# Kernel optimization log

Hardware: AMD Instinct MI355X
Metric: run time of the kernel (lower is better)

## Reference

```python
import jax, jax.numpy as jnp
import numpy as np

B, T, N, H = 256, 128, 512, 128  # batch, timesteps, input_size (driving series), hidden


def setup_inputs() -> dict:
    key = jax.random.key(0)
    ks = jax.random.split(key, 7)
    p = lambda k, shape: (jax.random.normal(k, shape, dtype=jnp.float32) * 0.05)
    return {
        "X": jax.random.normal(ks[0], (B, T, N), dtype=jnp.float32),
        # attention linear: in_features = 2H + T, out_features = 1 (stored as a vector + scalar bias)
        "attn_w": p(ks[1], (2 * H + T,)),
        "attn_b": p(ks[2], ()),
        # LSTM cell params, PyTorch layout/gate order (i, f, g, o)
        "w_ih": p(ks[3], (4 * H, N)),
        "w_hh": p(ks[4], (4 * H, H)),
        "b_ih": p(ks[5], (4 * H,)),
        "b_hh": p(ks[6], (4 * H,)),
    }


def reference(X, attn_w, attn_b, w_ih, w_hh, b_ih, b_hh):
    Bn, Tn, Nn = X.shape
    Hh = w_hh.shape[1]
    # split the single attention weight row into the h / s / X-row pieces of the concat
    w_h, w_s, w_x = attn_w[:Hh], attn_w[Hh:2 * Hh], attn_w[2 * Hh:]
    Xp = jnp.swapaxes(X, 1, 2)            # [B, N, T]  (X.permute(0,2,1))
    x_score = Xp @ w_x                    # [B, N], time-invariant part of attention logits

    def step(carry, x_t):                 # x_t: [B, N] = X[:, t, :]
        h, c = carry
        # logits[b,i] = w_h.h[b] + w_s.c[b] + w_x.Xp[b,i] + b  (== Linear on the concat)
        score = x_score + (h @ w_h + c @ w_s + attn_b)[:, None]   # [B, N]
        alpha = jax.nn.softmax(score, axis=1)
        x_tilde = alpha * x_t                                      # [B, N]
        gates = x_tilde @ w_ih.T + h @ w_hh.T + b_ih + b_hh        # [B, 4H]
        i, f, g, o = jnp.split(gates, 4, axis=1)
        c_new = jax.nn.sigmoid(f) * c + jax.nn.sigmoid(i) * jnp.tanh(g)
        h_new = jax.nn.sigmoid(o) * jnp.tanh(c_new)
        return (h_new, c_new), (x_tilde, h_new)

    h0 = jnp.zeros((Bn, Hh), X.dtype)
    (_, _), (Xt, Xe) = jax.lax.scan(step, (h0, h0), jnp.swapaxes(X, 0, 1))
    # scan stacks along time -> [T, B, .]; return [B, T, .]
    return jnp.swapaxes(Xt, 0, 1), jnp.swapaxes(Xe, 0, 1)
```

## Files before the change

### kernel.cpp

```cpp
#include <hip/hip_runtime.h>
#include <hip/hip_bf16.h>

#define Bb 256
#define Tt 128
#define Nn 512
#define Hh 128

typedef __attribute__((ext_vector_type(4))) float floatx4;
typedef __attribute__((ext_vector_type(8))) short short8;

__device__ __forceinline__ unsigned short f2bf(float f) {
  unsigned u = __float_as_uint(f);
  u += 0x7fffu + ((u >> 16) & 1u);
  return (unsigned short)(u >> 16);
}

__device__ __forceinline__ float sigmoid_fast(float x) {
  return __builtin_amdgcn_rcpf(1.f + __expf(-x));
}
__device__ __forceinline__ float tanh_fast(float x) {
  float e = __expf(2.f * x);
  return 1.f - 2.f * __builtin_amdgcn_rcpf(e + 1.f);
}

__device__ __forceinline__ void lds_barrier() {
  asm volatile("s_waitcnt lgkmcnt(0)" ::: "memory");
  __builtin_amdgcn_s_barrier();
  asm volatile("" ::: "memory");
}

__device__ __forceinline__ void async_load16(const void* g, void* lds) {
  __builtin_amdgcn_global_load_lds(
      (const __attribute__((address_space(1))) unsigned int*)g,
      (__attribute__((address_space(3))) unsigned int*)lds, 16, 0, 0);
}

__global__ void prep_kernel(const float* __restrict__ w_ih,
                            const float* __restrict__ b_ih,
                            const float* __restrict__ b_hh,
                            unsigned short* __restrict__ wb,
                            float* __restrict__ bias) {
  int i = blockIdx.x * 256 + threadIdx.x;
  if (i < 4 * Hh * Nn) wb[i] = f2bf(w_ih[i]);
  if (i < 4 * Hh) bias[i] = b_ih[i] + b_hh[i];
}

__global__ __launch_bounds__(512) void alpha_kernel(const float* __restrict__ X,
                                                    const float* __restrict__ attn_w,
                                                    float* __restrict__ alpha) {
  int b = blockIdx.x;
  int n = threadIdx.x;
  const float* Xb = X + (size_t)b * Tt * Nn + n;
  float acc = 0.f;
#pragma unroll 8
  for (int t = 0; t < Tt; ++t)
    acc = fmaf(Xb[(size_t)t * Nn], attn_w[2 * Hh + t], acc);

  __shared__ float red[512];
  red[n] = acc;
  __syncthreads();
  for (int s = 256; s > 0; s >>= 1) {
    if (n < s) red[n] = fmaxf(red[n], red[n + s]);
    __syncthreads();
  }
  float m = red[0];
  __syncthreads();
  float e = __expf(acc - m);
  red[n] = e;
  __syncthreads();
  for (int s = 256; s > 0; s >>= 1) {
    if (n < s) red[n] += red[n + s];
    __syncthreads();
  }
  alpha[(size_t)b * Nn + n] = e / red[0];
}

__global__ __launch_bounds__(256) void scale_kernel(const float* __restrict__ X,
                                                    const float* __restrict__ alpha,
                                                    float* __restrict__ Xt,
                                                    unsigned short* __restrict__ xtb) {
  size_t i = (size_t)blockIdx.x * 256 + threadIdx.x;
  size_t e = i * 4;
  int n = (int)(e & (Nn - 1));
  int brow = (int)(e >> 9);
  int b = brow >> 7;
  float4 x = ((const float4*)X)[i];
  float4 a = *(const float4*)(alpha + (size_t)b * Nn + n);
  float4 y;
  y.x = x.x * a.x; y.y = x.y * a.y; y.z = x.z * a.z; y.w = x.w * a.w;
  ((float4*)Xt)[i] = y;
  ushort4 u;
  u.x = f2bf(y.x); u.y = f2bf(y.y); u.z = f2bf(y.z); u.w = f2bf(y.w);
  ((ushort4*)xtb)[i] = u;
}

#define GBK 64

__global__ __launch_bounds__(256) void gemm_bt(const unsigned short* __restrict__ A,
                                               const unsigned short* __restrict__ Bw,
                                               const float* __restrict__ bias,
                                               float* __restrict__ C) {
  __shared__ __align__(16) unsigned short As[128 * 64];
  __shared__ __align__(16) unsigned short Bs[128 * 64];
  const int K = 512, NO = 512;
  int tid = threadIdx.x;
  int lane = tid & 63;
  int wave = tid >> 6;
  int wm = wave & 1, wn = wave >> 1;
  int l15 = lane & 15;
  int quad = lane >> 4;
  int mtile = blockIdx.x, ntile = blockIdx.y;

  floatx4 acc[4][4];
#pragma unroll
  for (int i = 0; i < 4; ++i)
#pragma unroll
    for (int j = 0; j < 4; ++j) acc[i][j] = (floatx4){0.f, 0.f, 0.f, 0.f};

  int lr = lane >> 3;
  int lc = (lane & 7) ^ lr;
  const size_t lane_goff = (size_t)lr * K + lc * 8;
  const size_t abase = (size_t)mtile * 128 * K + lane_goff;
  const size_t bbase = (size_t)ntile * 128 * K + lane_goff;
  int sw = (quad ^ (l15 & 7)) * 8;

  for (int kb = 0; kb < K; kb += GBK) {
#pragma unroll
    for (int slot = 0; slot < 4; ++slot) {
      int r0 = slot * 32 + wave * 8;
      async_load16(A + abase + (size_t)r0 * K + kb, &As[r0 * 64]);
      async_load16(Bw + bbase + (size_t)r0 * K + kb, &Bs[r0 * 64]);
    }
    __syncthreads();
#pragma unroll
    for (int kh = 0; kh < 2; ++kh) {
      int sc = sw ^ (kh * 32);
      short8 af[4], bf[4];
#pragma unroll
      for (int i = 0; i < 4; ++i)
        af[i] = *(const short8*)(&As[(wm * 64 + i * 16 + l15) * 64 + sc]);
#pragma unroll
      for (int j = 0; j < 4; ++j)
        bf[j] = *(const short8*)(&Bs[(wn * 64 + j * 16 + l15) * 64 + sc]);
#pragma unroll
      for (int i = 0; i < 4; ++i)
#pragma unroll
        for (int j = 0; j < 4; ++j)
          acc[i][j] = __builtin_amdgcn_mfma_f32_16x16x32_bf16(af[i], bf[j], acc[i][j], 0, 0, 0);
    }
    __syncthreads();
  }

  int m0 = mtile * 128 + wm * 64;
  int n0 = ntile * 128 + wn * 64;
#pragma unroll
  for (int j = 0; j < 4; ++j) {
    int col = n0 + j * 16 + l15;
    float bsum = bias[col];
#pragma unroll
    for (int i = 0; i < 4; ++i) {
      int row = m0 + i * 16 + quad * 4;
#pragma unroll
      for (int r = 0; r < 4; ++r)
        C[(size_t)(row + r) * NO + col] = acc[i][j][r] + bsum;
    }
  }
}

__global__ __launch_bounds__(512, 1) void lstm_kernel(const float* __restrict__ G,
                                                      const float* __restrict__ w_hh,
                                                      float* __restrict__ Xe) {
  int b = blockIdx.x;
  int tid = threadIdx.x;
  int w = tid >> 6;
  int lane = tid & 63;
  int l15 = lane & 15;
  int quad = lane >> 4;

  short8 bfr[4][4];
#pragma unroll
  for (int f = 0; f < 4; ++f) {
    int n = f * 128 + w * 16 + l15;
    const float* src = w_hh + (size_t)n * 128;
#pragma unroll
    for (int kf = 0; kf < 4; ++kf) {
      int k0 = kf * 32 + quad * 8;
      float4 lo = *(const float4*)(src + k0);
      float4 hi = *(const float4*)(src + k0 + 4);
      short8 v;
      v[0] = (short)f2bf(lo.x); v[1] = (short)f2bf(lo.y);
      v[2] = (short)f2bf(lo.z); v[3] = (short)f2bf(lo.w);
      v[4] = (short)f2bf(hi.x); v[5] = (short)f2bf(hi.y);
      v[6] = (short)f2bf(hi.z); v[7] = (short)f2bf(hi.w);
      bfr[f][kf] = v;
    }
  }

  __shared__ __align__(16) unsigned short h_sh[2][128];
  if (tid < 128) h_sh[0][tid] = 0;
  __syncthreads();

  const float* Gb = G + (size_t)b * Tt * 512;
  float* Xeb = Xe + (size_t)b * Tt * Hh;

  int goff[4];
#pragma unroll
  for (int f = 0; f < 4; ++f) goff[f] = f * 128 + w * 16 + l15;

  float gcur[4], gnext[4];
#pragma unroll
  for (int f = 0; f < 4; ++f) gcur[f] = Gb[goff[f]];
#pragma unroll
  for (int f = 0; f < 4; ++f) gnext[f] = Gb[512 + goff[f]];

  float c0 = 0.f;
  int j0 = w * 16 + l15;

  for (int t = 0; t < Tt; ++t) {
    int cur = t & 1;
    const unsigned short* hp = h_sh[cur];
    short8 af[4];
#pragma unroll
    for (int kf = 0; kf < 4; ++kf)
      af[kf] = *(const short8*)(hp + kf * 32 + quad * 8);

    floatx4 acc[4];
#pragma unroll
    for (int f = 0; f < 4; ++f)
      acc[f] = (floatx4){gcur[f], gcur[f], gcur[f], gcur[f]};

#pragma unroll
    for (int f = 0; f < 4; ++f) gcur[f] = gnext[f];
    if (t + 2 < Tt) {
      const float* Gt2 = Gb + (size_t)(t + 2) * 512;
#pragma unroll
      for (int f = 0; f < 4; ++f) gnext[f] = Gt2[goff[f]];
    }

#pragma unroll
    for (int kf = 0; kf < 4; ++kf)
#pragma unroll
      for (int f = 0; f < 4; ++f)
        acc[f] = __builtin_amdgcn_mfma_f32_16x16x32_bf16(af[kf], bfr[f][kf], acc[f], 0, 0, 0);

    float si = sigmoid_fast(acc[0][0]);
    float sf = sigmoid_fast(acc[1][0]);
    float tg = tanh_fast(acc[2][0]);
    float so = sigmoid_fast(acc[3][0]);

    c0 = sf * c0 + si * tg;
    float hv = so * tanh_fast(c0);

    if (quad == 0) {
      Xeb[(size_t)t * Hh + j0] = hv;
      h_sh[cur ^ 1][j0] = f2bf(hv);
    }
    lds_barrier();
  }
}

extern "C" void kernel_launch(void* const* d_in, const int* in_sizes, int n_in,
                              void* d_out, int out_size, void* d_ws, size_t ws_size,
                              hipStream_t stream) {
  const float* X      = (const float*)d_in[0];
  const float* attn_w = (const float*)d_in[1];
  const float* w_ih   = (const float*)d_in[3];
  const float* w_hh   = (const float*)d_in[4];
  const float* b_ih   = (const float*)d_in[5];
  const float* b_hh   = (const float*)d_in[6];

  float* Xt = (float*)d_out;
  float* Xe = (float*)d_out + (size_t)Bb * Tt * Nn;

  char* ws = (char*)d_ws;
  float*          alpha = (float*)(ws);
  float*          bias  = (float*)(ws + 524288);
  unsigned short* wb    = (unsigned short*)(ws + 526336);
  unsigned short* xtb   = (unsigned short*)(ws + 1050624);
  float*          G     = (float*)(ws + 34605056);

  prep_kernel<<<dim3(1024), dim3(256), 0, stream>>>(w_ih, b_ih, b_hh, wb, bias);
  alpha_kernel<<<dim3(Bb), dim3(512), 0, stream>>>(X, attn_w, alpha);
  scale_kernel<<<dim3(16384), dim3(256), 0, stream>>>(X, alpha, Xt, xtb);
  gemm_bt<<<dim3(256, 4), dim3(256), 0, stream>>>(xtb, wb, bias, G);
  lstm_kernel<<<dim3(Bb), dim3(512), 0, stream>>>(G, w_hh, Xe);
}
```

Baseline: 276.9 us.

## Replace MFMA recurrent matvec with fp16 dot2 and quad DPP reduction

```diff
diff --git a/kernel.cpp b/kernel.cpp
--- a/kernel.cpp
+++ b/kernel.cpp
@@ -8,6 +8,7 @@
 
 typedef __attribute__((ext_vector_type(4))) float floatx4;
 typedef __attribute__((ext_vector_type(8))) short short8;
+typedef _Float16 h2v_t __attribute__((ext_vector_type(2)));
 
 __device__ __forceinline__ unsigned short f2bf(float f) {
   unsigned u = __float_as_uint(f);
@@ -33,6 +34,25 @@
   __builtin_amdgcn_global_load_lds(
       (const __attribute__((address_space(1))) unsigned int*)g,
       (__attribute__((address_space(3))) unsigned int*)lds, 16, 0, 0);
+}
+
+#if __has_builtin(__builtin_amdgcn_fdot2)
+#define FDOT2(a, b, c) __builtin_amdgcn_fdot2((a), (b), (c), false)
+#else
+__device__ __forceinline__ float fdot2_sw(h2v_t a, h2v_t b, float c) {
+  return fmaf((float)a.x, (float)b.x, fmaf((float)a.y, (float)b.y, (c)));
+}
+#define FDOT2(a, b, c) fdot2_sw((a), (b), (c))
+#endif
+
+template <int CTRL>
+__device__ __forceinline__ float qperm(float x) {
+#if __has_builtin(__builtin_amdgcn_update_dpp)
+  return __uint_as_float((unsigned)__builtin_amdgcn_update_dpp(
+      0, (int)__float_as_uint(x), CTRL, 0xf, 0xf, true));
+#else
+  return __shfl_xor(x, CTRL == 0xB1 ? 1 : 2, 64);
+#endif
 }
 
 __global__ void prep_kernel(const float* __restrict__ w_ih,
@@ -172,88 +192,75 @@
                                                       float* __restrict__ Xe) {
   int b = blockIdx.x;
   int tid = threadIdx.x;
-  int w = tid >> 6;
-  int lane = tid & 63;
-  int l15 = lane & 15;
-  int quad = lane >> 4;
-
-  short8 bfr[4][4];
+  int u = tid >> 2;
+  int q = tid & 3;
+
+  h2v_t wreg[4][16];
 #pragma unroll
   for (int f = 0; f < 4; ++f) {
-    int n = f * 128 + w * 16 + l15;
-    const float* src = w_hh + (size_t)n * 128;
-#pragma unroll
-    for (int kf = 0; kf < 4; ++kf) {
-      int k0 = kf * 32 + quad * 8;
-      float4 lo = *(const float4*)(src + k0);
-      float4 hi = *(const float4*)(src + k0 + 4);
-      short8 v;
-      v[0] = (short)f2bf(lo.x); v[1] = (short)f2bf(lo.y);
-      v[2] = (short)f2bf(lo.z); v[3] = (short)f2bf(lo.w);
-      v[4] = (short)f2bf(hi.x); v[5] = (short)f2bf(hi.y);
-      v[6] = (short)f2bf(hi.z); v[7] = (short)f2bf(hi.w);
-      bfr[f][kf] = v;
-    }
-  }
-
-  __shared__ __align__(16) unsigned short h_sh[2][128];
-  if (tid < 128) h_sh[0][tid] = 0;
-  __syncthreads();
-
-  const float* Gb = G + (size_t)b * Tt * 512;
+    const float4* wr = (const float4*)(w_hh + ((size_t)(f * 128 + u) * 128 + q * 32));
+#pragma unroll
+    for (int i = 0; i < 8; ++i) {
+      float4 v = wr[i];
+      wreg[f][2 * i]     = (h2v_t){(_Float16)v.x, (_Float16)v.y};
+      wreg[f][2 * i + 1] = (h2v_t){(_Float16)v.z, (_Float16)v.w};
+    }
+  }
+
+  __shared__ __align__(16) unsigned short h2[2][128];
+  if (tid < 128) h2[0][tid] = 0;
+  __syncthreads();
+
+  const float* Gb = G + (size_t)b * Tt * 512 + q * 128 + u;
   float* Xeb = Xe + (size_t)b * Tt * Hh;
 
-  int goff[4];
-#pragma unroll
-  for (int f = 0; f < 4; ++f) goff[f] = f * 128 + w * 16 + l15;
-
-  float gcur[4], gnext[4];
-#pragma unroll
-  for (int f = 0; f < 4; ++f) gcur[f] = Gb[goff[f]];
-#pragma unroll
-  for (int f = 0; f < 4; ++f) gnext[f] = Gb[512 + goff[f]];
-
+  float gcur = Gb[0];
+  float gnext = Gb[512];
   float c0 = 0.f;
-  int j0 = w * 16 + l15;
 
   for (int t = 0; t < Tt; ++t) {
     int cur = t & 1;
-    const unsigned short* hp = h_sh[cur];
-    short8 af[4];
-#pragma unroll
-    for (int kf = 0; kf < 4; ++kf)
-      af[kf] = *(const short8*)(hp + kf * 32 + quad * 8);
-
-    floatx4 acc[4];
-#pragma unroll
-    for (int f = 0; f < 4; ++f)
-      acc[f] = (floatx4){gcur[f], gcur[f], gcur[f], gcur[f]};
-
-#pragma unroll
-    for (int f = 0; f < 4; ++f) gcur[f] = gnext[f];
-    if (t + 2 < Tt) {
-      const float* Gt2 = Gb + (size_t)(t + 2) * 512;
-#pragma unroll
-      for (int f = 0; f < 4; ++f) gnext[f] = Gt2[goff[f]];
-    }
-
-#pragma unroll
-    for (int kf = 0; kf < 4; ++kf)
-#pragma unroll
-      for (int f = 0; f < 4; ++f)
-        acc[f] = __builtin_amdgcn_mfma_f32_16x16x32_bf16(af[kf], bfr[f][kf], acc[f], 0, 0, 0);
-
-    float si = sigmoid_fast(acc[0][0]);
-    float sf = sigmoid_fast(acc[1][0]);
-    float tg = tanh_fast(acc[2][0]);
-    float so = sigmoid_fast(acc[3][0]);
-
+    const uint4* hp = (const uint4*)(&h2[cur][0]) + q * 4;
+    uint4 ha = hp[0], hb = hp[1], hc = hp[2], hd = hp[3];
+
+    float g_this = gcur;
+    gcur = gnext;
+    if (t + 2 < Tt) gnext = Gb[(size_t)(t + 2) * 512];
+
+    float pg0 = (q == 0) ? g_this : 0.f;
+    float pg1 = (q == 1) ? g_this : 0.f;
+    float pg2 = (q == 2) ? g_this : 0.f;
+    float pg3 = (q == 3) ? g_this : 0.f;
+
+#define DOTK(HB, K2)                                                \
+  {                                                                 \
+    h2v_t hh = __builtin_bit_cast(h2v_t, (HB));                     \
+    pg0 = FDOT2(hh, wreg[0][K2], pg0);                              \
+    pg1 = FDOT2(hh, wreg[1][K2], pg1);                              \
+    pg2 = FDOT2(hh, wreg[2][K2], pg2);                              \
+    pg3 = FDOT2(hh, wreg[3][K2], pg3);                              \
+  }
+    DOTK(ha.x, 0)  DOTK(ha.y, 1)  DOTK(ha.z, 2)  DOTK(ha.w, 3)
+    DOTK(hb.x, 4)  DOTK(hb.y, 5)  DOTK(hb.z, 6)  DOTK(hb.w, 7)
+    DOTK(hc.x, 8)  DOTK(hc.y, 9)  DOTK(hc.z, 10) DOTK(hc.w, 11)
+    DOTK(hd.x, 12) DOTK(hd.y, 13) DOTK(hd.z, 14) DOTK(hd.w, 15)
+#undef DOTK
+
+    pg0 += qperm<0xB1>(pg0); pg1 += qperm<0xB1>(pg1);
+    pg2 += qperm<0xB1>(pg2); pg3 += qperm<0xB1>(pg3);
+    pg0 += qperm<0x4E>(pg0); pg1 += qperm<0x4E>(pg1);
+    pg2 += qperm<0x4E>(pg2); pg3 += qperm<0x4E>(pg3);
+
+    float si = sigmoid_fast(pg0);
+    float sf = sigmoid_fast(pg1);
+    float tg = tanh_fast(pg2);
+    float so = sigmoid_fast(pg3);
     c0 = sf * c0 + si * tg;
     float hv = so * tanh_fast(c0);
 
-    if (quad == 0) {
-      Xeb[(size_t)t * Hh + j0] = hv;
-      h_sh[cur ^ 1][j0] = f2bf(hv);
+    if (q == 0) {
+      Xeb[(size_t)t * Hh + u] = hv;
+      h2[cur ^ 1][u] = __builtin_bit_cast(unsigned short, (_Float16)hv);
     }
     lds_barrier();
   }
```

Result: no change. 274.0 us (-1.1%).
